# Optimization experiments

Measured on AMD Instinct MI355X. Metric: run time of the kernel, lower is better.

The kernel has to match this reference:

```python
import jax, jax.numpy as jnp
import numpy as np

B, N_N, N_A, D = 1024, 96, 96, 512


def _normalize(x):
    return x / jnp.linalg.norm(x, axis=-1, keepdims=True)


def setup_inputs() -> dict:
    key = jax.random.key(0)
    ks = jax.random.split(key, 8)
    img_embs = _normalize(jax.random.normal(ks[0], (B, D), jnp.float32))
    normal_text_embs = _normalize(jax.random.normal(ks[1], (N_N, D), jnp.float32))
    abnormal_text_embs = _normalize(jax.random.normal(ks[2], (N_A, D), jnp.float32))
    logit_scale = jnp.full((1,), np.log(100.0), jnp.float32)  # CLIP temperature
    W1 = jax.random.normal(ks[3], (2 * D, D), jnp.float32) / np.sqrt(2 * D)
    b1 = jnp.zeros((D,), jnp.float32)
    W2 = jax.random.normal(ks[4], (D, D // 2), jnp.float32) / np.sqrt(D)
    b2 = jnp.zeros((D // 2,), jnp.float32)
    W3 = jax.random.normal(ks[5], (D // 2, D // 4), jnp.float32) / np.sqrt(D // 2)
    b3 = jnp.zeros((D // 4,), jnp.float32)
    return {"img_embs": img_embs, "normal_text_embs": normal_text_embs,
            "abnormal_text_embs": abnormal_text_embs, "logit_scale": logit_scale,
            "W1": W1, "b1": b1, "W2": W2, "b2": b2, "W3": W3, "b3": b3}


def _mlp(x, W1, b1, W2, b2, W3, b3):
    h = jax.nn.relu(x @ W1 + b1)
    h = jax.nn.relu(h @ W2 + b2)
    return h @ W3 + b3


def _branch(img_embs, text_embs, scale, W1, b1, W2, b2, W3, b3):
    # sims: [B, N]; softmax weights then exp-scaled text embeddings
    sims = (img_embs @ text_embs.T) * scale
    w = jax.nn.softmax(sims, axis=-1)
    scaled_text = text_embs[None, :, :] * jnp.exp(w)[:, :, None]      # [B, N, D]
    rep_img = jnp.broadcast_to(img_embs[:, None, :], scaled_text.shape)  # [B, N, D]
    x = jnp.concatenate([rep_img, scaled_text], axis=-1)              # [B, N, 2D]
    h = _mlp(x, W1, b1, W2, b2, W3, b3)                               # [B, N, D//4]
    return h.mean(axis=1)                                             # [B, D//4]


def reference(img_embs, normal_text_embs, abnormal_text_embs, logit_scale,
              W1, b1, W2, b2, W3, b3):
    scale = jnp.exp(logit_scale[0])
    h_n = _branch(img_embs, normal_text_embs, scale, W1, b1, W2, b2, W3, b3)
    h_a = _branch(img_embs, abnormal_text_embs, scale, W1, b1, W2, b2, W3, b3)
    return (h_n, h_a)
```

## Files before the change

### kernel.cpp

```cpp
#include <hip/hip_runtime.h>
#include <hip/hip_bf16.h>


typedef __attribute__((ext_vector_type(8))) short short8;
typedef __attribute__((ext_vector_type(4))) float floatx4;
typedef __attribute__((ext_vector_type(4))) unsigned int uint4v;

__device__ __forceinline__ unsigned short f2bf(float x) {
    unsigned int u = __float_as_uint(x);
    u += 0x7fffu + ((u >> 16) & 1u);
    return (unsigned short)(u >> 16);
}
__device__ __forceinline__ float bf2f(unsigned short u) {
    return __uint_as_float(((unsigned int)u) << 16);
}

template <bool BF16OUT>
__device__ __forceinline__ void gemm32(
    const float* __restrict__ A0, const float* __restrict__ A1, int rows0,
    const float* __restrict__ Bm, float* __restrict__ Cf,
    unsigned short* __restrict__ Cb, int mt, int nt, float* sAT, int t) {
    int r0 = mt * 32, c0 = nt * 64;
    int rg = t >> 4, cg = t & 15;
    int lrow = t >> 3, k4 = (t & 7) * 4;
    int gr = r0 + lrow;
    const float* Ap = (gr < rows0) ? (A0 + gr * 512) : (A1 + (gr - rows0) * 512);
    float acc[2][4];
#pragma unroll
    for (int r = 0; r < 2; r++)
#pragma unroll
        for (int c = 0; c < 4; c++) acc[r][c] = 0.f;
    const float* Bp = Bm + c0 + cg * 4;
    for (int k0 = 0; k0 < 512; k0 += 32) {
        __syncthreads();
        float4 av = *(const float4*)(Ap + k0 + k4);
        sAT[(k4 + 0) * 34 + lrow] = av.x;
        sAT[(k4 + 1) * 34 + lrow] = av.y;
        sAT[(k4 + 2) * 34 + lrow] = av.z;
        sAT[(k4 + 3) * 34 + lrow] = av.w;
        __syncthreads();
#pragma unroll 8
        for (int kk = 0; kk < 32; kk++) {
            float a0 = sAT[kk * 34 + rg * 2];
            float a1 = sAT[kk * 34 + rg * 2 + 1];
            float4 bv = *(const float4*)(Bp + (k0 + kk) * 512);
            acc[0][0] = fmaf(a0, bv.x, acc[0][0]); acc[0][1] = fmaf(a0, bv.y, acc[0][1]);
            acc[0][2] = fmaf(a0, bv.z, acc[0][2]); acc[0][3] = fmaf(a0, bv.w, acc[0][3]);
            acc[1][0] = fmaf(a1, bv.x, acc[1][0]); acc[1][1] = fmaf(a1, bv.y, acc[1][1]);
            acc[1][2] = fmaf(a1, bv.z, acc[1][2]); acc[1][3] = fmaf(a1, bv.w, acc[1][3]);
        }
    }
    int rr = r0 + rg * 2, cc = c0 + cg * 4;
#pragma unroll
    for (int r = 0; r < 2; r++) {
        if (BF16OUT) {
            unsigned long long pk =
                (unsigned long long)f2bf(acc[r][0]) | ((unsigned long long)f2bf(acc[r][1]) << 16) |
                ((unsigned long long)f2bf(acc[r][2]) << 32) | ((unsigned long long)f2bf(acc[r][3]) << 48);
            *(unsigned long long*)(Cb + (rr + r) * 512 + cc) = pk;
        } else {
            *(float4*)(Cf + (rr + r) * 512 + cc) = make_float4(acc[r][0], acc[r][1], acc[r][2], acc[r][3]);
        }
    }
}

__global__ __launch_bounds__(256) void prep_kernel(
    const float* __restrict__ img, const float* __restrict__ tn,
    const float* __restrict__ ta, const float* __restrict__ ls,
    const float* __restrict__ W1, const float* __restrict__ W2,
    float* __restrict__ e_ws, float* __restrict__ U_ws,
    unsigned short* __restrict__ Tb, unsigned short* __restrict__ W2T) {
    __shared__ __align__(16) float smem[8704];
    int idx = blockIdx.x;
    int t = threadIdx.x;

    if (idx < 256) {
        int bi0 = idx * 4;
        float* sImg = smem;
        float* sS   = smem + 2064;
        float* sMx  = smem + 2832;
        float* sSum = smem + 2840;
#pragma unroll
        for (int p = 0; p < 2; p++) {
            int i4 = t + 256 * p;
            int i = i4 >> 7, k4 = (i4 & 127) * 4;
            float4 v = *(const float4*)(img + (bi0 + i) * 512 + k4);
            sImg[i * 516 + k4 + 0] = v.x; sImg[i * 516 + k4 + 1] = v.y;
            sImg[i * 516 + k4 + 2] = v.z; sImg[i * 516 + k4 + 3] = v.w;
        }
        __syncthreads();
        float scale = __expf(ls[0]);
        int i = t & 3, n0 = (t >> 2) * 3;
        const float* txp[3];
#pragma unroll
        for (int r = 0; r < 3; r++) {
            int n = n0 + r;
            txp[r] = (n < 96) ? (tn + n * 512) : (ta + (n - 96) * 512);
        }
        float d0 = 0.f, d1 = 0.f, d2 = 0.f;
        const float* ib = &sImg[i * 516];
#pragma unroll 4
        for (int k4 = 0; k4 < 512; k4 += 4) {
            float4 iv = *(const float4*)(ib + k4);
            float4 a = *(const float4*)(txp[0] + k4);
            float4 b = *(const float4*)(txp[1] + k4);
            float4 c = *(const float4*)(txp[2] + k4);
            d0 += iv.x * a.x + iv.y * a.y + iv.z * a.z + iv.w * a.w;
            d1 += iv.x * b.x + iv.y * b.y + iv.z * b.z + iv.w * b.w;
            d2 += iv.x * c.x + iv.y * c.y + iv.z * c.z + iv.w * c.w;
        }
        sS[i * 192 + n0 + 0] = d0 * scale;
        sS[i * 192 + n0 + 1] = d1 * scale;
        sS[i * 192 + n0 + 2] = d2 * scale;
        __syncthreads();
        if (t < 8) {
            int ii = t >> 1, brx = t & 1;
            const float* base = &sS[ii * 192 + brx * 96];
            float m = -1e30f;
            for (int n = 0; n < 96; n++) m = fmaxf(m, base[n]);
            float s = 0.f;
            for (int n = 0; n < 96; n++) s += __expf(base[n] - m);
            sMx[t] = m; sSum[t] = s;
        }
        __syncthreads();
#pragma unroll
        for (int p = 0; p < 3; p++) {
            int j = t + 256 * p;
            int ii = j & 3, n = j >> 2;
            int brx = (n >= 96) ? 1 : 0;
            int nn = n - brx * 96;
            float w = __expf(sS[ii * 192 + n] - sMx[ii * 2 + brx]) / sSum[ii * 2 + brx];
            e_ws[(brx * 1024 + bi0 + ii) * 96 + nn] = __expf(w);
        }
    } else if (idx < 512) {
        int i2 = idx - 256;
        gemm32<false>(img, img, 1 << 20, W1, U_ws, nullptr, i2 >> 3, i2 & 7, smem, t);
    } else if (idx < 560) {
        int i2 = idx - 512;
        gemm32<true>(tn, ta, 96, W1 + 512 * 512, nullptr, Tb, i2 >> 3, i2 & 7, smem, t);
    } else {
        int ci = idx - 560;
        int k0 = ci * 32;
        float* sWT = smem;
        int kr = t >> 3, n0 = (t & 7) * 32;
#pragma unroll
        for (int c = 0; c < 8; c++) {
            float4 v = *(const float4*)(W2 + (k0 + kr) * 256 + n0 + c * 4);
            sWT[(n0 + c * 4 + 0) * 33 + kr] = v.x;
            sWT[(n0 + c * 4 + 1) * 33 + kr] = v.y;
            sWT[(n0 + c * 4 + 2) * 33 + kr] = v.z;
            sWT[(n0 + c * 4 + 3) * 33 + kr] = v.w;
        }
        __syncthreads();
        unsigned short pk[32];
#pragma unroll
        for (int k = 0; k < 32; k++) pk[k] = f2bf(sWT[t * 33 + k]);
#pragma unroll
        for (int g = 0; g < 4; g++) {
            uint4v u;
#pragma unroll
            for (int c = 0; c < 4; c++)
                u[c] = (unsigned int)pk[g * 8 + 2 * c] | ((unsigned int)pk[g * 8 + 2 * c + 1] << 16);
            *(uint4v*)(W2T + t * 512 + k0 + g * 8) = u;
        }
    }
}

__global__ __launch_bounds__(512, 4) void branch_mlp5(
    const float* __restrict__ U, const unsigned short* __restrict__ Tb,
    const float* __restrict__ e_all, const unsigned short* __restrict__ W2T,
    const float* __restrict__ b1, const float* __restrict__ b2,
    const float* __restrict__ W3, const float* __restrict__ b3,
    float* __restrict__ out) {
    int b = blockIdx.x, br = blockIdx.y;
    const unsigned short* T = Tb + br * (96 * 512);

    __shared__ float sUb[512];
    __shared__ float sE[96];
    __shared__ __align__(16) unsigned short sH[2][96][88];
    __shared__ float sM2[256];
    __shared__ float sPart[512];

    int t = threadIdx.x;
    sUb[t] = U[b * 512 + t] + b1[t];
    if (t < 96) sE[t] = e_all[(br * 1024 + b) * 96 + t];
    __syncthreads();

    const int wave = t >> 6, lane = t & 63;
    const int frow = lane & 15, fkq = (lane >> 4) * 8;
    const int ncol0 = wave * 32;
    const int srow = t >> 3;
    const int skc = (t & 7) * 8;
    const bool two = (srow < 32);

    const floatx4 fz = {0.f, 0.f, 0.f, 0.f};
    floatx4 acc[6][2];
#pragma unroll
    for (int mt = 0; mt < 6; mt++) {
        acc[mt][0] = fz; acc[mt][1] = fz;
    }

    int trow1 = srow + 64;
    float ev0 = sE[srow], ev1 = two ? sE[trow1] : 0.f;
    short8 tv0 = *(const short8*)(T + srow * 512 + skc);
    short8 tv1 = two ? *(const short8*)(T + trow1 * 512 + skc) : tv0;

    const unsigned short* Bbase = W2T + (ncol0 + frow) * 512 + fkq;
    short8 bpre[2];
    bpre[0] = *(const short8*)(Bbase);
    bpre[1] = *(const short8*)(Bbase + 16 * 512);

#pragma unroll
    for (int s = 0; s < 8; s++) {
        int k0 = s * 64;
        float4 u0 = *(const float4*)(&sUb[k0 + skc]);
        float4 u1 = *(const float4*)(&sUb[k0 + skc + 4]);
        float ua[8] = {u0.x, u0.y, u0.z, u0.w, u1.x, u1.y, u1.z, u1.w};
        {
            uint4v pk;
#pragma unroll
            for (int jj = 0; jj < 4; jj++) {
                float f0 = fmaxf(fmaf(ev0, bf2f((unsigned short)tv0[2 * jj]), ua[2 * jj]), 0.f);
                float f1 = fmaxf(fmaf(ev0, bf2f((unsigned short)tv0[2 * jj + 1]), ua[2 * jj + 1]), 0.f);
                __hip_bfloat162 h2 = __float22bfloat162_rn(make_float2(f0, f1));
                unsigned int bits; __builtin_memcpy(&bits, &h2, 4);
                pk[jj] = bits;
            }
            *(uint4v*)(&sH[s & 1][srow][skc]) = pk;
        }
        if (two) {
            uint4v pk;
#pragma unroll
            for (int jj = 0; jj < 4; jj++) {
                float f0 = fmaxf(fmaf(ev1, bf2f((unsigned short)tv1[2 * jj]), ua[2 * jj]), 0.f);
                float f1 = fmaxf(fmaf(ev1, bf2f((unsigned short)tv1[2 * jj + 1]), ua[2 * jj + 1]), 0.f);
                __hip_bfloat162 h2 = __float22bfloat162_rn(make_float2(f0, f1));
                unsigned int bits; __builtin_memcpy(&bits, &h2, 4);
                pk[jj] = bits;
            }
            *(uint4v*)(&sH[s & 1][trow1][skc]) = pk;
        }
        short8 bcur0 = bpre[0], bcur1 = bpre[1];
        if (s < 7) {
            tv0 = *(const short8*)(T + srow * 512 + k0 + 64 + skc);
            if (two) tv1 = *(const short8*)(T + trow1 * 512 + k0 + 64 + skc);
            bpre[0] = *(const short8*)(Bbase + k0 + 64);
            bpre[1] = *(const short8*)(Bbase + 16 * 512 + k0 + 64);
        }
        __syncthreads();
        short8 b1f0 = *(const short8*)(Bbase + k0 + 32);
        short8 b1f1 = *(const short8*)(Bbase + 16 * 512 + k0 + 32);
#pragma unroll
        for (int mt = 0; mt < 6; mt++) {
            short8 afr = *(const short8*)(&sH[s & 1][mt * 16 + frow][fkq]);
            acc[mt][0] = __builtin_amdgcn_mfma_f32_16x16x32_bf16(afr, bcur0, acc[mt][0], 0, 0, 0);
            acc[mt][1] = __builtin_amdgcn_mfma_f32_16x16x32_bf16(afr, bcur1, acc[mt][1], 0, 0, 0);
        }
#pragma unroll
        for (int mt = 0; mt < 6; mt++) {
            short8 afr = *(const short8*)(&sH[s & 1][mt * 16 + frow][32 + fkq]);
            acc[mt][0] = __builtin_amdgcn_mfma_f32_16x16x32_bf16(afr, b1f0, acc[mt][0], 0, 0, 0);
            acc[mt][1] = __builtin_amdgcn_mfma_f32_16x16x32_bf16(afr, b1f1, acc[mt][1], 0, 0, 0);
        }
    }

#pragma unroll
    for (int j = 0; j < 2; j++) {
        int col = ncol0 + j * 16 + frow;
        float bb = b2[col];
        float s = 0.f;
#pragma unroll
        for (int mt = 0; mt < 6; mt++)
#pragma unroll
            for (int r = 0; r < 4; r++)
                s += fmaxf(acc[mt][j][r] + bb, 0.f);
        s += __shfl_xor(s, 16);
        s += __shfl_xor(s, 32);
        if (lane < 16) sM2[col] = s * (1.0f / 96.0f);
    }
    __syncthreads();

    int col = t & 127, kq = t >> 7;
    const float* w3p = W3 + (kq * 64) * 128 + col;
    const float* mp = sM2 + kq * 64;
    float o = 0.f;
#pragma unroll 8
    for (int k = 0; k < 64; k++) o = fmaf(mp[k], w3p[k * 128], o);
    sPart[t] = o;
    __syncthreads();
    if (t < 128)
        out[(br * 1024 + b) * 128 + t] =
            sPart[t] + sPart[t + 128] + sPart[t + 256] + sPart[t + 384] + b3[t];
}

extern "C" void kernel_launch(void* const* d_in, const int* in_sizes, int n_in,
                              void* d_out, int out_size, void* d_ws, size_t ws_size,
                              hipStream_t stream) {
    const float* img = (const float*)d_in[0];
    const float* tn  = (const float*)d_in[1];
    const float* ta  = (const float*)d_in[2];
    const float* ls  = (const float*)d_in[3];
    const float* W1  = (const float*)d_in[4];
    const float* b1  = (const float*)d_in[5];
    const float* W2  = (const float*)d_in[6];
    const float* b2  = (const float*)d_in[7];
    const float* W3  = (const float*)d_in[8];
    const float* b3  = (const float*)d_in[9];
    float* out = (float*)d_out;
    float* ws  = (float*)d_ws;

    float* e_ws = ws;
    float* U_ws = ws + 196608;
    unsigned short* Tb  = (unsigned short*)(ws + 720896);
    unsigned short* W2T = (unsigned short*)(ws + 770048);

    prep_kernel<<<576, 256, 0, stream>>>(img, tn, ta, ls, W1, W2, e_ws, U_ws, Tb, W2T);
    branch_mlp5<<<dim3(1024, 2), 512, 0, stream>>>(U_ws, Tb, e_ws, W2T, b1, b2, W3, b3, out);
}
```

Measured before the change: 212.9 us.

## Split branch MLP over text-row halves, pre-swizzle W2 fragments, separate output GEMV

```diff
diff --git a/kernel.cpp b/kernel.cpp
--- a/kernel.cpp
+++ b/kernel.cpp
@@ -69,7 +69,7 @@
     const float* __restrict__ ta, const float* __restrict__ ls,
     const float* __restrict__ W1, const float* __restrict__ W2,
     float* __restrict__ e_ws, float* __restrict__ U_ws,
-    unsigned short* __restrict__ Tb, unsigned short* __restrict__ W2T) {
+    unsigned short* __restrict__ Tb, unsigned short* __restrict__ W2Tf) {
     __shared__ __align__(16) float smem[8704];
     int idx = blockIdx.x;
     int t = threadIdx.x;
@@ -139,8 +139,8 @@
         int i2 = idx - 512;
         gemm32<true>(tn, ta, 96, W1 + 512 * 512, nullptr, Tb, i2 >> 3, i2 & 7, smem, t);
     } else {
-        int ci = idx - 560;
-        int k0 = ci * 32;
+        int kt = idx - 560;
+        int k0 = kt * 32;
         float* sWT = smem;
         int kr = t >> 3, n0 = (t & 7) * 32;
 #pragma unroll
@@ -152,70 +152,76 @@
             sWT[(n0 + c * 4 + 3) * 33 + kr] = v.w;
         }
         __syncthreads();
-        unsigned short pk[32];
-#pragma unroll
-        for (int k = 0; k < 32; k++) pk[k] = f2bf(sWT[t * 33 + k]);
-#pragma unroll
-        for (int g = 0; g < 4; g++) {
+        int lane = t & 63;
+        int kl = (lane >> 4) * 8;
+#pragma unroll
+        for (int it = 0; it < 4; it++) {
+            int nt = it * 4 + (t >> 6);
+            int n = nt * 16 + (lane & 15);
             uint4v u;
 #pragma unroll
-            for (int c = 0; c < 4; c++)
-                u[c] = (unsigned int)pk[g * 8 + 2 * c] | ((unsigned int)pk[g * 8 + 2 * c + 1] << 16);
-            *(uint4v*)(W2T + t * 512 + k0 + g * 8) = u;
-        }
-    }
-}
-
-__global__ __launch_bounds__(512, 4) void branch_mlp5(
+            for (int c = 0; c < 4; c++) {
+                unsigned short lo = f2bf(sWT[n * 33 + kl + 2 * c]);
+                unsigned short hi = f2bf(sWT[n * 33 + kl + 2 * c + 1]);
+                u[c] = (unsigned int)lo | ((unsigned int)hi << 16);
+            }
+            *(uint4v*)(W2Tf + (((kt * 16 + nt) * 64) + lane) * 8) = u;
+        }
+    }
+}
+
+__global__ __launch_bounds__(256, 4) void branch_mlp6(
     const float* __restrict__ U, const unsigned short* __restrict__ Tb,
-    const float* __restrict__ e_all, const unsigned short* __restrict__ W2T,
+    const float* __restrict__ e_all, const unsigned short* __restrict__ W2Tf,
     const float* __restrict__ b1, const float* __restrict__ b2,
-    const float* __restrict__ W3, const float* __restrict__ b3,
-    float* __restrict__ out) {
-    int b = blockIdx.x, br = blockIdx.y;
-    const unsigned short* T = Tb + br * (96 * 512);
+    float* __restrict__ m2p) {
+    int b = blockIdx.x, br = blockIdx.y, half = blockIdx.z;
+    const unsigned short* T = Tb + br * (96 * 512) + half * (48 * 512);
 
     __shared__ float sUb[512];
-    __shared__ float sE[96];
-    __shared__ __align__(16) unsigned short sH[2][96][88];
-    __shared__ float sM2[256];
-    __shared__ float sPart[512];
+    __shared__ float sE[48];
+    __shared__ __align__(16) unsigned short sH[2][48 * 64];
 
     int t = threadIdx.x;
     sUb[t] = U[b * 512 + t] + b1[t];
-    if (t < 96) sE[t] = e_all[(br * 1024 + b) * 96 + t];
+    sUb[t + 256] = U[b * 512 + t + 256] + b1[t + 256];
+    if (t < 48) sE[t] = e_all[(br * 1024 + b) * 96 + half * 48 + t];
     __syncthreads();
 
     const int wave = t >> 6, lane = t & 63;
     const int frow = lane & 15, fkq = (lane >> 4) * 8;
-    const int ncol0 = wave * 32;
+    const int f7 = frow & 7;
     const int srow = t >> 3;
     const int skc = (t & 7) * 8;
-    const bool two = (srow < 32);
+    const bool two = (t < 128);
+    const int srow2 = 32 + (t >> 3);
 
     const floatx4 fz = {0.f, 0.f, 0.f, 0.f};
-    floatx4 acc[6][2];
-#pragma unroll
-    for (int mt = 0; mt < 6; mt++) {
-        acc[mt][0] = fz; acc[mt][1] = fz;
-    }
-
-    int trow1 = srow + 64;
-    float ev0 = sE[srow], ev1 = two ? sE[trow1] : 0.f;
-    short8 tv0 = *(const short8*)(T + srow * 512 + skc);
-    short8 tv1 = two ? *(const short8*)(T + trow1 * 512 + skc) : tv0;
-
-    const unsigned short* Bbase = W2T + (ncol0 + frow) * 512 + fkq;
-    short8 bpre[2];
-    bpre[0] = *(const short8*)(Bbase);
-    bpre[1] = *(const short8*)(Bbase + 16 * 512);
+    floatx4 acc[3][4];
+#pragma unroll
+    for (int mt = 0; mt < 3; mt++)
+#pragma unroll
+        for (int j = 0; j < 4; j++) acc[mt][j] = fz;
+
+    float ev0 = sE[srow];
+    float ev1 = two ? sE[srow2] : 0.f;
+    const int sw1 = skc ^ ((srow & 7) * 8);
+    const int sw2 = skc ^ ((srow2 & 7) * 8);
+
+    const unsigned short* Wf = W2Tf + (wave * 4 * 64 + lane) * 8;
+    short8 bpre[4];
+#pragma unroll
+    for (int j = 0; j < 4; j++)
+        bpre[j] = *(const short8*)(Wf + j * (64 * 8));
 
 #pragma unroll
     for (int s = 0; s < 8; s++) {
         int k0 = s * 64;
+        unsigned short* sHb = sH[s & 1];
         float4 u0 = *(const float4*)(&sUb[k0 + skc]);
         float4 u1 = *(const float4*)(&sUb[k0 + skc + 4]);
         float ua[8] = {u0.x, u0.y, u0.z, u0.w, u1.x, u1.y, u1.z, u1.w};
+        short8 tv0 = *(const short8*)(T + srow * 512 + k0 + skc);
         {
             uint4v pk;
 #pragma unroll
@@ -226,9 +232,10 @@
                 unsigned int bits; __builtin_memcpy(&bits, &h2, 4);
                 pk[jj] = bits;
             }
-            *(uint4v*)(&sH[s & 1][srow][skc]) = pk;
+            *(uint4v*)(&sHb[srow * 64 + sw1]) = pk;
         }
         if (two) {
+            short8 tv1 = *(const short8*)(T + srow2 * 512 + k0 + skc);
             uint4v pk;
 #pragma unroll
             for (int jj = 0; jj < 4; jj++) {
@@ -238,59 +245,68 @@
                 unsigned int bits; __builtin_memcpy(&bits, &h2, 4);
                 pk[jj] = bits;
             }
-            *(uint4v*)(&sH[s & 1][trow1][skc]) = pk;
-        }
-        short8 bcur0 = bpre[0], bcur1 = bpre[1];
+            *(uint4v*)(&sHb[srow2 * 64 + sw2]) = pk;
+        }
+        __syncthreads();
+        short8 b1f[4];
+#pragma unroll
+        for (int j = 0; j < 4; j++)
+            b1f[j] = *(const short8*)(Wf + ((2 * s + 1) * 16 + j) * (64 * 8));
+        const int ka0 = (((fkq >> 3) ^ f7) << 3);
+        const int ka1 = (((4 + (fkq >> 3)) ^ f7) << 3);
+#pragma unroll
+        for (int mt = 0; mt < 3; mt++) {
+            short8 afr = *(const short8*)(&sHb[(mt * 16 + frow) * 64 + ka0]);
+#pragma unroll
+            for (int j = 0; j < 4; j++)
+                acc[mt][j] = __builtin_amdgcn_mfma_f32_16x16x32_bf16(afr, bpre[j], acc[mt][j], 0, 0, 0);
+        }
         if (s < 7) {
-            tv0 = *(const short8*)(T + srow * 512 + k0 + 64 + skc);
-            if (two) tv1 = *(const short8*)(T + trow1 * 512 + k0 + 64 + skc);
-            bpre[0] = *(const short8*)(Bbase + k0 + 64);
-            bpre[1] = *(const short8*)(Bbase + 16 * 512 + k0 + 64);
-        }
-        __syncthreads();
-        short8 b1f0 = *(const short8*)(Bbase + k0 + 32);
-        short8 b1f1 = *(const short8*)(Bbase + 16 * 512 + k0 + 32);
-#pragma unroll
-        for (int mt = 0; mt < 6; mt++) {
-            short8 afr = *(const short8*)(&sH[s & 1][mt * 16 + frow][fkq]);
-            acc[mt][0] = __builtin_amdgcn_mfma_f32_16x16x32_bf16(afr, bcur0, acc[mt][0], 0, 0, 0);
-            acc[mt][1] = __builtin_amdgcn_mfma_f32_16x16x32_bf16(afr, bcur1, acc[mt][1], 0, 0, 0);
-        }
-#pragma unroll
-        for (int mt = 0; mt < 6; mt++) {
-            short8 afr = *(const short8*)(&sH[s & 1][mt * 16 + frow][32 + fkq]);
-            acc[mt][0] = __builtin_amdgcn_mfma_f32_16x16x32_bf16(afr, b1f0, acc[mt][0], 0, 0, 0);
-            acc[mt][1] = __builtin_amdgcn_mfma_f32_16x16x32_bf16(afr, b1f1, acc[mt][1], 0, 0, 0);
-        }
-    }
-
-#pragma unroll
-    for (int j = 0; j < 2; j++) {
-        int col = ncol0 + j * 16 + frow;
+#pragma unroll
+            for (int j = 0; j < 4; j++)
+                bpre[j] = *(const short8*)(Wf + ((2 * s + 2) * 16 + j) * (64 * 8));
+        }
+#pragma unroll
+        for (int mt = 0; mt < 3; mt++) {
+            short8 afr = *(const short8*)(&sHb[(mt * 16 + frow) * 64 + ka1]);
+#pragma unroll
+            for (int j = 0; j < 4; j++)
+                acc[mt][j] = __builtin_amdgcn_mfma_f32_16x16x32_bf16(afr, b1f[j], acc[mt][j], 0, 0, 0);
+        }
+    }
+
+#pragma unroll
+    for (int j = 0; j < 4; j++) {
+        int col = wave * 64 + j * 16 + frow;
         float bb = b2[col];
         float s = 0.f;
 #pragma unroll
-        for (int mt = 0; mt < 6; mt++)
+        for (int mt = 0; mt < 3; mt++)
 #pragma unroll
             for (int r = 0; r < 4; r++)
                 s += fmaxf(acc[mt][j][r] + bb, 0.f);
         s += __shfl_xor(s, 16);
         s += __shfl_xor(s, 32);
-        if (lane < 16) sM2[col] = s * (1.0f / 96.0f);
-    }
+        if (lane < 16)
+            m2p[(((half * 2 + br) * 1024) + b) * 256 + col] = s;
+    }
+}
+
+__global__ __launch_bounds__(128) void out_kernel(
+    const float* __restrict__ m2p, const float* __restrict__ W3,
+    const float* __restrict__ b3, float* __restrict__ out) {
+    int b = blockIdx.x, br = blockIdx.y;
+    int t = threadIdx.x;
+    __shared__ float sM[256];
+    const float* p0 = m2p + ((0 + br) * 1024 + b) * 256;
+    const float* p1 = m2p + ((2 + br) * 1024 + b) * 256;
+    sM[t]       = (p0[t]       + p1[t])       * (1.0f / 96.0f);
+    sM[t + 128] = (p0[t + 128] + p1[t + 128]) * (1.0f / 96.0f);
     __syncthreads();
-
-    int col = t & 127, kq = t >> 7;
-    const float* w3p = W3 + (kq * 64) * 128 + col;
-    const float* mp = sM2 + kq * 64;
-    float o = 0.f;
+    float o = b3[t];
 #pragma unroll 8
-    for (int k = 0; k < 64; k++) o = fmaf(mp[k], w3p[k * 128], o);
-    sPart[t] = o;
-    __syncthreads();
-    if (t < 128)
-        out[(br * 1024 + b) * 128 + t] =
-            sPart[t] + sPart[t + 128] + sPart[t + 256] + sPart[t + 384] + b3[t];
+    for (int k = 0; k < 256; k++) o = fmaf(sM[k], W3[k * 128 + t], o);
+    out[(br * 1024 + b) * 128 + t] = o;
 }
 
 extern "C" void kernel_launch(void* const* d_in, const int* in_sizes, int n_in,
@@ -311,9 +327,11 @@
 
     float* e_ws = ws;
     float* U_ws = ws + 196608;
-    unsigned short* Tb  = (unsigned short*)(ws + 720896);
-    unsigned short* W2T = (unsigned short*)(ws + 770048);
-
-    prep_kernel<<<576, 256, 0, stream>>>(img, tn, ta, ls, W1, W2, e_ws, U_ws, Tb, W2T);
-    branch_mlp5<<<dim3(1024, 2), 512, 0, stream>>>(U_ws, Tb, e_ws, W2T, b1, b2, W3, b3, out);
-}
+    unsigned short* Tb   = (unsigned short*)(ws + 720896);
+    unsigned short* W2Tf = (unsigned short*)(ws + 770048);
+    float* m2p = ws + 835584;
+
+    prep_kernel<<<576, 256, 0, stream>>>(img, tn, ta, ls, W1, W2, e_ws, U_ws, Tb, W2Tf);
+    branch_mlp6<<<dim3(1024, 2, 2), 256, 0, stream>>>(U_ws, Tb, e_ws, W2Tf, b1, b2, m2p);
+    out_kernel<<<dim3(1024, 2), 128, 0, stream>>>(m2p, W3, b3, out);
+}
```

New measurement: 193.3 us. -9.2%, faster.
